# Kernel optimization log

Measured on AMD Instinct MI355X. Metric: run time of the kernel, lower is better.

Reference implementation:

```python
import jax, jax.numpy as jnp
import numpy as np

B, L, D, H = 4, 2048, 1024, 16
HD = D // H

def setup_inputs() -> dict:
    key = jax.random.key(0)
    ks = jax.random.split(key, 11)
    s = 1.0 / np.sqrt(D)
    return {
        "query": jax.random.normal(ks[0], (B, L, D), jnp.float32),
        "key": jax.random.normal(ks[1], (B, L, D), jnp.float32),
        "value": jax.random.normal(ks[2], (B, L, D), jnp.float32),
        "Wq": jax.random.normal(ks[3], (D, D), jnp.float32) * s,
        "bq": jnp.zeros((D,), jnp.float32),
        "Wk": jax.random.normal(ks[4], (D, D), jnp.float32) * s,
        "bk": jnp.zeros((D,), jnp.float32),
        "Wv": jax.random.normal(ks[5], (D, D), jnp.float32) * s,
        "bv": jnp.zeros((D,), jnp.float32),
        "Wo": jax.random.normal(ks[6], (D, D), jnp.float32) * s,
        "bo": jnp.zeros((D,), jnp.float32),
    }

def reference(query, key, value, Wq, bq, Wk, bk, Wv, bv, Wo, bo):
    b = query.shape[0]
    # linear projections (torch Linear: x @ W.T + b)
    Q = query @ Wq.T + bq
    K = key @ Wk.T + bk
    V = value @ Wv.T + bv
    # split heads -> [b, h, l, hd]
    Q = Q.reshape(b, -1, H, HD).transpose(0, 2, 1, 3)
    K = K.reshape(b, -1, H, HD).transpose(0, 2, 1, 3)
    V = V.reshape(b, -1, H, HD).transpose(0, 2, 1, 3)
    energy = jnp.einsum('bhqd,bhkd->bhqk', Q, K) / jnp.sqrt(jnp.float32(HD))
    attn = jax.nn.softmax(energy, axis=-1)
    x = jnp.einsum('bhqk,bhkd->bhqd', attn, V)
    x = x.transpose(0, 2, 1, 3).reshape(b, -1, D)
    return x @ Wo.T + bo
```

## Files before the change

kernel.cpp:

```cpp
#include <hip/hip_runtime.h>

typedef float floatx4 __attribute__((ext_vector_type(4)));
typedef short bf16x8 __attribute__((ext_vector_type(8)));
typedef const unsigned int __attribute__((address_space(1))) gas_u32;
typedef unsigned int __attribute__((address_space(3))) las_u32;

#if __has_builtin(__builtin_amdgcn_exp2f)
#define EXP2F(x) __builtin_amdgcn_exp2f(x)
#else
#define EXP2F(x) exp2f(x)
#endif

__device__ __forceinline__ unsigned short f2bf(float x) {
    unsigned int u = __float_as_uint(x);
    unsigned int r = u + 0x7fffu + ((u >> 16) & 1u);
    return (unsigned short)(r >> 16);
}

__device__ __forceinline__ unsigned int pack2bf_t(float lo, float hi) {
    return (__float_as_uint(lo) >> 16) | (__float_as_uint(hi) & 0xffff0000u);
}

__device__ __forceinline__ void g2l16(const void* g, void* l) {
    __builtin_amdgcn_global_load_lds((gas_u32*)(unsigned long long)g,
                                     (las_u32*)(unsigned int)(unsigned long long)l,
                                     16, 0, 0);
}

__global__ __launch_bounds__(256) void cvt5_kernel(
    const float* __restrict__ k, const float* __restrict__ v,
    const float* __restrict__ wq, const float* __restrict__ wk, const float* __restrict__ wv,
    unsigned short* __restrict__ kb, unsigned short* __restrict__ vb,
    unsigned short* __restrict__ wqb, unsigned short* __restrict__ wkb,
    unsigned short* __restrict__ wvb) {
    const int ty = blockIdx.y;
    const float* src; unsigned short* dst; int n4;
    switch (ty) {
        case 0: src = k;  dst = kb;  n4 = 2097152; break;
        case 1: src = v;  dst = vb;  n4 = 2097152; break;
        case 2: src = wq; dst = wqb; n4 = 262144;  break;
        case 3: src = wk; dst = wkb; n4 = 262144;  break;
        default: src = wv; dst = wvb; n4 = 262144; break;
    }
    int i = blockIdx.x * 256 + threadIdx.x;
    if (i >= n4) return;
    float4 x = ((const float4*)src)[i];
    ushort4 o;
    o.x = f2bf(x.x); o.y = f2bf(x.y); o.z = f2bf(x.z); o.w = f2bf(x.w);
    ((ushort4*)dst)[i] = o;
}

__global__ __launch_bounds__(256) void cvt1_kernel(const float* __restrict__ wo,
                                                   unsigned short* __restrict__ wob) {
    int i = blockIdx.x * 256 + threadIdx.x;
    float4 x = ((const float4*)wo)[i];
    ushort4 o;
    o.x = f2bf(x.x); o.y = f2bf(x.y); o.z = f2bf(x.z); o.w = f2bf(x.w);
    ((ushort4*)wob)[i] = o;
}

template <int OUT_MODE, bool A_FP32>
__device__ __forceinline__ void gemm_body(const void* __restrict__ Aptr,
                                          const unsigned short* __restrict__ W,
                                          const float* __restrict__ bias,
                                          void* __restrict__ Cout,
                                          unsigned short* As, unsigned short* Bs,
                                          int m0, int n0, int N, int K, float scale) {
    const int t = threadIdx.x;
    const int lane = t & 63, w = t >> 6;
    const int lr = lane & 15, quad = lane >> 4;
    const int wm = (w & 1) * 64, wn = (w >> 1) * 64;

    const int s0 = w * 128 + lane, s1 = s0 + 64;
    const int r0 = s0 >> 2, c0 = ((s0 & 3) ^ (r0 & 3)) * 8;
    const int r1 = s1 >> 2, c1 = ((s1 & 3) ^ (r1 & 3)) * 8;
    const unsigned short* gw0 = W + (size_t)(n0 + r0) * K + c0;
    const unsigned short* gw1 = W + (size_t)(n0 + r1) * K + c1;

    const unsigned short* ga0 = nullptr;
    const unsigned short* ga1 = nullptr;
    if constexpr (!A_FP32) {
        const unsigned short* A = (const unsigned short*)Aptr;
        ga0 = A + (size_t)(m0 + r0) * K + c0;
        ga1 = A + (size_t)(m0 + r1) * K + c1;
    }

    floatx4 acc[4][4];
#pragma unroll
    for (int i = 0; i < 4; ++i)
#pragma unroll
        for (int j = 0; j < 4; ++j) acc[i][j] = (floatx4){0.f, 0.f, 0.f, 0.f};

    const int xs = (lr & 3);

    auto stage = [&](int buf, int k0) {
        unsigned short* Ab = As + buf * 4096;
        unsigned short* Bb = Bs + buf * 4096;
        g2l16(gw0 + k0, &Bb[(size_t)(w * 128) * 8]);
        g2l16(gw1 + k0, &Bb[(size_t)(w * 128 + 64) * 8]);
        if constexpr (A_FP32) {
            const float* A = (const float*)Aptr;
            float4 v[4];
#pragma unroll
            for (int i = 0; i < 4; ++i) {
                int idx = t + 256 * i;
                int row = idx >> 3;
                int c4 = (idx & 7) * 4;
                v[i] = *(const float4*)(A + (size_t)(m0 + row) * K + k0 + c4);
            }
#pragma unroll
            for (int i = 0; i < 4; ++i) {
                int idx = t + 256 * i;
                int row = idx >> 3;
                int c4 = (idx & 7) * 4;
                ushort4 bv;
                bv.x = f2bf(v[i].x); bv.y = f2bf(v[i].y);
                bv.z = f2bf(v[i].z); bv.w = f2bf(v[i].w);
                *(ushort4*)&Ab[row * 32 + c4] = bv;
            }
        } else {
            g2l16(ga0 + k0, &Ab[(size_t)(w * 128) * 8]);
            g2l16(ga1 + k0, &Ab[(size_t)(w * 128 + 64) * 8]);
        }
    };

    auto compute = [&](int buf) {
        const unsigned short* Ab = As + buf * 4096;
        const unsigned short* Bb = Bs + buf * 4096;
        bf16x8 af[4], bfr[4];
#pragma unroll
        for (int i = 0; i < 4; ++i) {
            int ch = A_FP32 ? quad : (quad ^ xs);
            af[i] = *(const bf16x8*)&Ab[(wm + i * 16 + lr) * 32 + ch * 8];
        }
#pragma unroll
        for (int j = 0; j < 4; ++j)
            bfr[j] = *(const bf16x8*)&Bb[(wn + j * 16 + lr) * 32 + ((quad ^ xs) * 8)];
#pragma unroll
        for (int i = 0; i < 4; ++i)
#pragma unroll
            for (int j = 0; j < 4; ++j) {
                if constexpr (OUT_MODE == 2)
                    acc[i][j] = __builtin_amdgcn_mfma_f32_16x16x32_bf16(bfr[j], af[i], acc[i][j], 0, 0, 0);
                else
                    acc[i][j] = __builtin_amdgcn_mfma_f32_16x16x32_bf16(af[i], bfr[j], acc[i][j], 0, 0, 0);
            }
    };

    stage(0, 0);
    __syncthreads();
    for (int k0 = 0; k0 < K - 64; k0 += 64) {
        stage(1, k0 + 32);
        compute(0);
        __syncthreads();
        stage(0, k0 + 64);
        compute(1);
        __syncthreads();
    }
    stage(1, K - 32);
    compute(0);
    __syncthreads();
    compute(1);

    if constexpr (OUT_MODE == 2) {
        const int b = m0 >> 11;
        unsigned short* VT = (unsigned short*)Cout;
#pragma unroll
        for (int i = 0; i < 4; ++i) {
#pragma unroll
            for (int j = 0; j < 4; ++j) {
#pragma unroll
                for (int r = 0; r < 4; ++r) {
                    int d = n0 + wn + j * 16 + quad * 4 + r;
                    int tok = (m0 & 2047) + wm + i * 16 + lr;
                    float val = acc[i][j][r] + bias[d];
                    int t6 = tok & 63;
                    int ntok = (tok & ~63) | ((((t6 >> 3) ^ (d & 7)) << 3)) | (t6 & 7);
                    VT[(((size_t)b * 16 + (d >> 6)) * 64 + (d & 63)) * 2048 + ntok] = f2bf(val);
                }
            }
        }
    } else if constexpr (OUT_MODE == 3) {
        unsigned short* C = (unsigned short*)Cout;
#pragma unroll
        for (int i = 0; i < 4; ++i) {
#pragma unroll
            for (int j = 0; j < 4; ++j) {
#pragma unroll
                for (int r = 0; r < 4; ++r) {
                    int row = m0 + wm + i * 16 + quad * 4 + r;
                    int col = n0 + wn + j * 16 + lr;
                    float val = acc[i][j][r] + bias[col];
                    int r6 = row & 63;
                    int srow = (r6 & 32) | (((r6 >> 2) & 1) << 4) |
                               (((r6 >> 3) & 3) << 2) | (r6 & 3);
                    int nrow = (row & ~63) | srow;
                    int c6 = col & 63;
                    int ncol = (col & ~63) | ((((c6 >> 3) ^ (srow & 7)) << 3)) | (c6 & 7);
                    C[(size_t)nrow * N + ncol] = f2bf(val);
                }
            }
        }
    } else {
#pragma unroll
        for (int i = 0; i < 4; ++i) {
#pragma unroll
            for (int j = 0; j < 4; ++j) {
#pragma unroll
                for (int r = 0; r < 4; ++r) {
                    int row = m0 + wm + i * 16 + quad * 4 + r;
                    int col = n0 + wn + j * 16 + lr;
                    float val = (acc[i][j][r] + bias[col]) * scale;
                    if constexpr (OUT_MODE == 1)
                        ((unsigned short*)Cout)[(size_t)row * N + col] = f2bf(val);
                    else
                        ((float*)Cout)[(size_t)row * N + col] = val;
                }
            }
        }
    }
}

__device__ __forceinline__ void gemm_swz(int bx, int by, int& m0, int& n0) {
    const int hw = bx + 8 * by;
    const int wid = (hw & 7) * 64 + (hw >> 3);
    m0 = (wid >> 3) * 128;
    n0 = (wid & 7) * 128;
}

__global__ __launch_bounds__(256) void gemm_qkv(
    const float* __restrict__ query, const unsigned short* __restrict__ wqb,
    const float* __restrict__ bq, unsigned short* __restrict__ Qp,
    const unsigned short* __restrict__ kb, const unsigned short* __restrict__ wkb,
    const float* __restrict__ bk, unsigned short* __restrict__ Kp,
    const unsigned short* __restrict__ vb, const unsigned short* __restrict__ wvb,
    const float* __restrict__ bv, unsigned short* __restrict__ VTp, float qscale) {
    __shared__ unsigned short As[2 * 128 * 32];
    __shared__ unsigned short Bs[2 * 128 * 32];
    int m0, n0;
    gemm_swz(blockIdx.x, blockIdx.y, m0, n0);
    if (blockIdx.z == 0)
        gemm_body<1, true>(query, wqb, bq, Qp, As, Bs, m0, n0, 1024, 1024, qscale);
    else if (blockIdx.z == 1)
        gemm_body<3, false>(kb, wkb, bk, Kp, As, Bs, m0, n0, 1024, 1024, 1.0f);
    else
        gemm_body<2, false>(vb, wvb, bv, VTp, As, Bs, m0, n0, 1024, 1024, 1.0f);
}

__global__ __launch_bounds__(256) void gemm_o(const unsigned short* __restrict__ A,
                                              const unsigned short* __restrict__ W,
                                              const float* __restrict__ bias,
                                              void* __restrict__ C) {
    __shared__ unsigned short As[2 * 128 * 32];
    __shared__ unsigned short Bs[2 * 128 * 32];
    int m0, n0;
    gemm_swz(blockIdx.x, blockIdx.y, m0, n0);
    gemm_body<0, false>(A, W, bias, C, As, Bs, m0, n0, 1024, 1024, 1.0f);
}

__global__ __launch_bounds__(256) void attn_kernel(const unsigned short* __restrict__ Qp,
                                                   const unsigned short* __restrict__ Kp,
                                                   const unsigned short* __restrict__ VTp,
                                                   unsigned short* __restrict__ Xp) {
    constexpr int L = 2048, D = 1024;
    __shared__ unsigned short Ks[2][64 * 64];
    __shared__ unsigned short Vt[2][64 * 64];

    const int t = threadIdx.x;
    const int hw = blockIdx.x + 16 * blockIdx.y + 256 * blockIdx.z;
    const int wid = (hw & 7) * 128 + (hw >> 3);
    const int q0 = (wid & 15) * 128;
    const int h = (wid >> 4) & 15;
    const int b = wid >> 8;
    const int lane = t & 63;
    const int w = t >> 6;
    const int lr = lane & 15;
    const int quad = lane >> 4;
    const int x7 = lr & 7;

    const size_t kbase = ((size_t)(b * L)) * D + (size_t)h * 64;
    const size_t vtbase = ((size_t)(b * 16 + h)) * 64 * 2048;

    auto stage_async = [&](int buf, int kb2) {
        int k0 = kb2 * 64;
#pragma unroll
        for (int i = 0; i < 2; ++i) {
            int idx = t + 256 * i;
            int row = idx >> 3, c16 = idx & 7;
            g2l16(Kp + kbase + (size_t)(k0 + row) * D + c16 * 8,
                  &Ks[buf][(w * 64 + i * 256) * 8]);
            g2l16(VTp + vtbase + (size_t)row * 2048 + k0 + c16 * 8,
                  &Vt[buf][(w * 64 + i * 256) * 8]);
        }
    };

    stage_async(0, 0);

    const size_t qbase = ((size_t)(b * L + q0)) * D + (size_t)h * 64;
    bf16x8 bq[2][2];
#pragma unroll
    for (int qs = 0; qs < 2; ++qs)
#pragma unroll
        for (int s2 = 0; s2 < 2; ++s2)
            bq[qs][s2] = *(const bf16x8*)(Qp + qbase + (size_t)(w * 32 + qs * 16 + lr) * D +
                                          s2 * 32 + quad * 8);

    floatx4 o[2][4], ol[2];
#pragma unroll
    for (int qs = 0; qs < 2; ++qs) {
        ol[qs] = (floatx4){0.f, 0.f, 0.f, 0.f};
#pragma unroll
        for (int dt = 0; dt < 4; ++dt) o[qs][dt] = (floatx4){0.f, 0.f, 0.f, 0.f};
    }
    bf16x8 ones;
#pragma unroll
    for (int e = 0; e < 8; ++e) ones[e] = (short)0x3F80;

    __syncthreads();
    int cur = 0;

    const int kc0 = (quad ^ x7) * 8;
    const int kc1 = ((quad + 4) ^ x7) * 8;

    for (int kb = 0; kb < L / 64; ++kb) {
        if (kb < L / 64 - 1) stage_async(cur ^ 1, kb + 1);

        __builtin_amdgcn_s_setprio(1);
#pragma unroll
        for (int g = 0; g < 2; ++g) {
            bf16x8 akA0 = *(const bf16x8*)&Ks[cur][(g * 32 + lr) * 64 + kc0];
            bf16x8 akA1 = *(const bf16x8*)&Ks[cur][(g * 32 + lr) * 64 + kc1];
            bf16x8 akB0 = *(const bf16x8*)&Ks[cur][(g * 32 + 16 + lr) * 64 + kc0];
            bf16x8 akB1 = *(const bf16x8*)&Ks[cur][(g * 32 + 16 + lr) * 64 + kc1];
            bf16x8 vf[4];
#pragma unroll
            for (int dt = 0; dt < 4; ++dt)
                vf[dt] = *(const bf16x8*)&Vt[cur][(dt * 16 + lr) * 64 +
                                                  (((g * 4 + quad) ^ x7) * 8)];

            const floatx4 z4 = (floatx4){0.f, 0.f, 0.f, 0.f};
#pragma unroll
            for (int qs = 0; qs < 2; ++qs) {
                floatx4 stA = __builtin_amdgcn_mfma_f32_16x16x32_bf16(akA0, bq[qs][0], z4, 0, 0, 0);
                stA = __builtin_amdgcn_mfma_f32_16x16x32_bf16(akA1, bq[qs][1], stA, 0, 0, 0);
                floatx4 stB = __builtin_amdgcn_mfma_f32_16x16x32_bf16(akB0, bq[qs][0], z4, 0, 0, 0);
                stB = __builtin_amdgcn_mfma_f32_16x16x32_bf16(akB1, bq[qs][1], stB, 0, 0, 0);

                union { unsigned int u[4]; bf16x8 v; } pf;
                pf.u[0] = pack2bf_t(EXP2F(stA[0]), EXP2F(stA[1]));
                pf.u[1] = pack2bf_t(EXP2F(stA[2]), EXP2F(stA[3]));
                pf.u[2] = pack2bf_t(EXP2F(stB[0]), EXP2F(stB[1]));
                pf.u[3] = pack2bf_t(EXP2F(stB[2]), EXP2F(stB[3]));

                ol[qs] = __builtin_amdgcn_mfma_f32_16x16x32_bf16(pf.v, ones, ol[qs], 0, 0, 0);
#pragma unroll
                for (int dt = 0; dt < 4; ++dt)
                    o[qs][dt] = __builtin_amdgcn_mfma_f32_16x16x32_bf16(pf.v, vf[dt],
                                                                        o[qs][dt], 0, 0, 0);
            }
        }
        __builtin_amdgcn_s_setprio(0);

        if (kb < L / 64 - 1) {
            __syncthreads();
            cur ^= 1;
        }
    }

#pragma unroll
    for (int qs = 0; qs < 2; ++qs) {
#pragma unroll
        for (int r = 0; r < 4; ++r) {
            float inv = 1.0f / ol[qs][r];
            int q = q0 + w * 32 + qs * 16 + quad * 4 + r;
            size_t base = ((size_t)(b * L + q)) * D + (size_t)h * 64;
#pragma unroll
            for (int dt = 0; dt < 4; ++dt)
                Xp[base + dt * 16 + lr] = f2bf(o[qs][dt][r] * inv);
        }
    }
}

extern "C" void kernel_launch(void* const* d_in, const int* in_sizes, int n_in,
                              void* d_out, int out_size, void* d_ws, size_t ws_size,
                              hipStream_t stream) {
    const float* query = (const float*)d_in[0];
    const float* key_  = (const float*)d_in[1];
    const float* value = (const float*)d_in[2];
    const float* Wq = (const float*)d_in[3];
    const float* bq = (const float*)d_in[4];
    const float* Wk = (const float*)d_in[5];
    const float* bk = (const float*)d_in[6];
    const float* Wv = (const float*)d_in[7];
    const float* bv = (const float*)d_in[8];
    const float* Wo = (const float*)d_in[9];
    const float* bo = (const float*)d_in[10];
    float* out = (float*)d_out;

    const size_t MB16 = (size_t)8 * 1024 * 1024;

    unsigned short* Qp  = (unsigned short*)d_ws;
    unsigned short* kb  = Qp + MB16;
    unsigned short* vb  = kb + MB16;
    unsigned short* VTp = vb + MB16;
    unsigned short* Xp  = kb;
    unsigned short* wob = vb;
    unsigned short* Kp  = (unsigned short*)d_out;
    unsigned short* wqb = Kp + MB16;
    unsigned short* wkb = wqb + 1024 * 1024;
    unsigned short* wvb = wkb + 1024 * 1024;

    const float qscale = 0.125f * 1.44269504f;

    dim3 bb(256);
    cvt5_kernel<<<dim3(8192, 5), bb, 0, stream>>>(key_, value, Wq, Wk, Wv,
                                                  kb, vb, wqb, wkb, wvb);
    gemm_qkv<<<dim3(8, 64, 3), bb, 0, stream>>>(query, wqb, bq, Qp,
                                                kb, wkb, bk, Kp,
                                                vb, wvb, bv, VTp, qscale);
    attn_kernel<<<dim3(16, 16, 4), bb, 0, stream>>>(Qp, Kp, VTp, Xp);
    cvt1_kernel<<<dim3(1024), bb, 0, stream>>>(Wo, wob);
    gemm_o<<<dim3(8, 64), bb, 0, stream>>>(Xp, wob, bo, out);
}
```

Baseline: 345.5 us.

## Load bf16 A-operand fragments directly from global memory into registers in GEMMs

For the bf16-input GEMM paths (K/V projections and output projection), the A tile is no longer staged through LDS. Each wave reads its MFMA A fragments straight from global memory into registers, and only the weight (B) tile keeps using LDS double buffering. This removes LDS traffic and shared memory for A, which may raise occupancy for gemm_o, but it exposes global load latency on the MFMA path with no prefetch, and wave pairs that share rows load the same A data redundantly.

```diff
diff --git a/kernel.cpp b/kernel.cpp
--- a/kernel.cpp
+++ b/kernel.cpp
@@ -77,12 +77,12 @@
     const unsigned short* gw0 = W + (size_t)(n0 + r0) * K + c0;
     const unsigned short* gw1 = W + (size_t)(n0 + r1) * K + c1;
 
-    const unsigned short* ga0 = nullptr;
-    const unsigned short* ga1 = nullptr;
+    const unsigned short* gA0 = nullptr;
+    const unsigned short* gA1 = nullptr;
     if constexpr (!A_FP32) {
         const unsigned short* A = (const unsigned short*)Aptr;
-        ga0 = A + (size_t)(m0 + r0) * K + c0;
-        ga1 = A + (size_t)(m0 + r1) * K + c1;
+        gA0 = A + (size_t)(m0 + wm + lr) * K + quad * 8;
+        gA1 = A + (size_t)(m0 + wm + 32 + lr) * K + quad * 8;
     }
 
     floatx4 acc[4][4];
@@ -93,49 +93,36 @@
 
     const int xs = (lr & 3);
 
-    auto stage = [&](int buf, int k0) {
-        unsigned short* Ab = As + buf * 4096;
+    auto stageB = [&](int buf, int k0) {
         unsigned short* Bb = Bs + buf * 4096;
         g2l16(gw0 + k0, &Bb[(size_t)(w * 128) * 8]);
         g2l16(gw1 + k0, &Bb[(size_t)(w * 128 + 64) * 8]);
-        if constexpr (A_FP32) {
-            const float* A = (const float*)Aptr;
-            float4 v[4];
-#pragma unroll
-            for (int i = 0; i < 4; ++i) {
-                int idx = t + 256 * i;
-                int row = idx >> 3;
-                int c4 = (idx & 7) * 4;
-                v[i] = *(const float4*)(A + (size_t)(m0 + row) * K + k0 + c4);
-            }
-#pragma unroll
-            for (int i = 0; i < 4; ++i) {
-                int idx = t + 256 * i;
-                int row = idx >> 3;
-                int c4 = (idx & 7) * 4;
-                ushort4 bv;
-                bv.x = f2bf(v[i].x); bv.y = f2bf(v[i].y);
-                bv.z = f2bf(v[i].z); bv.w = f2bf(v[i].w);
-                *(ushort4*)&Ab[row * 32 + c4] = bv;
-            }
-        } else {
-            g2l16(ga0 + k0, &Ab[(size_t)(w * 128) * 8]);
-            g2l16(ga1 + k0, &Ab[(size_t)(w * 128 + 64) * 8]);
-        }
     };
 
-    auto compute = [&](int buf) {
-        const unsigned short* Ab = As + buf * 4096;
-        const unsigned short* Bb = Bs + buf * 4096;
-        bf16x8 af[4], bfr[4];
+    auto stageA32 = [&](int buf, int k0) {
+        unsigned short* Ab = As + buf * 4096;
+        const float* A = (const float*)Aptr;
+        float4 v[4];
 #pragma unroll
         for (int i = 0; i < 4; ++i) {
-            int ch = A_FP32 ? quad : (quad ^ xs);
-            af[i] = *(const bf16x8*)&Ab[(wm + i * 16 + lr) * 32 + ch * 8];
-        }
-#pragma unroll
-        for (int j = 0; j < 4; ++j)
-            bfr[j] = *(const bf16x8*)&Bb[(wn + j * 16 + lr) * 32 + ((quad ^ xs) * 8)];
+            int idx = t + 256 * i;
+            int row = idx >> 3;
+            int c4 = (idx & 7) * 4;
+            v[i] = *(const float4*)(A + (size_t)(m0 + row) * K + k0 + c4);
+        }
+#pragma unroll
+        for (int i = 0; i < 4; ++i) {
+            int idx = t + 256 * i;
+            int row = idx >> 3;
+            int c4 = (idx & 7) * 4;
+            ushort4 bv;
+            bv.x = f2bf(v[i].x); bv.y = f2bf(v[i].y);
+            bv.z = f2bf(v[i].z); bv.w = f2bf(v[i].w);
+            *(ushort4*)&Ab[row * 32 + c4] = bv;
+        }
+    };
+
+    auto mfma16 = [&](const bf16x8* af, const bf16x8* bfr) {
 #pragma unroll
         for (int i = 0; i < 4; ++i)
 #pragma unroll
@@ -147,20 +134,70 @@
             }
     };
 
-    stage(0, 0);
-    __syncthreads();
-    for (int k0 = 0; k0 < K - 64; k0 += 64) {
-        stage(1, k0 + 32);
-        compute(0);
+    auto readB = [&](int buf, bf16x8* bfr) {
+        const unsigned short* Bb = Bs + buf * 4096;
+#pragma unroll
+        for (int j = 0; j < 4; ++j)
+            bfr[j] = *(const bf16x8*)&Bb[(wn + j * 16 + lr) * 32 + ((quad ^ xs) * 8)];
+    };
+
+    if constexpr (!A_FP32) {
+        auto loadA = [&](bf16x8* af, int k0) {
+#pragma unroll
+            for (int i = 0; i < 2; ++i) {
+                af[i]     = *(const bf16x8*)(gA0 + (size_t)i * 16 * K + k0);
+                af[i + 2] = *(const bf16x8*)(gA1 + (size_t)i * 16 * K + k0);
+            }
+        };
+        auto step = [&](int buf, int k0) {
+            bf16x8 af[4], bfr[4];
+            loadA(af, k0);
+            readB(buf, bfr);
+            mfma16(af, bfr);
+        };
+        stageB(0, 0);
         __syncthreads();
-        stage(0, k0 + 64);
-        compute(1);
+        for (int k0 = 0; k0 < K - 64; k0 += 64) {
+            stageB(1, k0 + 32);
+            step(0, k0);
+            __syncthreads();
+            stageB(0, k0 + 64);
+            step(1, k0 + 32);
+            __syncthreads();
+        }
+        stageB(1, K - 32);
+        step(0, K - 64);
         __syncthreads();
-    }
-    stage(1, K - 32);
-    compute(0);
-    __syncthreads();
-    compute(1);
+        step(1, K - 32);
+    } else {
+        auto stepA32 = [&](int buf) {
+            const unsigned short* Ab = As + buf * 4096;
+            bf16x8 af[4], bfr[4];
+#pragma unroll
+            for (int i = 0; i < 4; ++i)
+                af[i] = *(const bf16x8*)&Ab[(wm + i * 16 + lr) * 32 + quad * 8];
+            readB(buf, bfr);
+            mfma16(af, bfr);
+        };
+        stageB(0, 0);
+        stageA32(0, 0);
+        __syncthreads();
+        for (int k0 = 0; k0 < K - 64; k0 += 64) {
+            stageB(1, k0 + 32);
+            stageA32(1, k0 + 32);
+            stepA32(0);
+            __syncthreads();
+            stageB(0, k0 + 64);
+            stageA32(0, k0 + 64);
+            stepA32(1);
+            __syncthreads();
+        }
+        stageB(1, K - 32);
+        stageA32(1, K - 32);
+        stepA32(0);
+        __syncthreads();
+        stepA32(1);
+    }
 
     if constexpr (OUT_MODE == 2) {
         const int b = m0 >> 11;
@@ -251,11 +288,10 @@
                                               const unsigned short* __restrict__ W,
                                               const float* __restrict__ bias,
                                               void* __restrict__ C) {
-    __shared__ unsigned short As[2 * 128 * 32];
     __shared__ unsigned short Bs[2 * 128 * 32];
     int m0, n0;
     gemm_swz(blockIdx.x, blockIdx.y, m0, n0);
-    gemm_body<0, false>(A, W, bias, C, As, Bs, m0, n0, 1024, 1024, 1.0f);
+    gemm_body<0, false>(A, W, bias, C, nullptr, Bs, m0, n0, 1024, 1024, 1.0f);
 }
 
 __global__ __launch_bounds__(256) void attn_kernel(const unsigned short* __restrict__ Qp,
```

Measured after the change: 396.2 us. +14.7%, slower.
